# Performance work log

Hardware: AMD Instinct MI355X
Metric: run time of the kernel (lower is better)

## Reference

```python
import jax, jax.numpy as jnp
import numpy as np

SIM_T = 0.2       # similarity_threshold
AMB_T = 0.17      # ambiguous_threshold
SPLIT = 24576     # split_size
CAP = 65536       # fixed capacity per split for compacted pairs (padded with -1)


def _l2norm(x):
    # F.normalize(p=2, dim=1) with eps clamp
    n = jnp.linalg.norm(x, axis=1, keepdims=True)
    return x / jnp.maximum(n, 1e-12)


def setup_inputs():
    key = jax.random.key(0)
    ks = jax.random.split(key, 8)
    N1, N2, D = 4096, 49152, 512
    features = jax.random.normal(ks[0], (N1, D), dtype=jnp.float32)
    labels = jax.random.randint(ks[1], (N1,), 0, 10000, dtype=jnp.int32)
    counts = jax.random.randint(ks[2], (N1,), 0, 100, dtype=jnp.int32)
    indexes = jax.random.randint(ks[3], (N1,), 0, N2, dtype=jnp.int32)
    features_db = jax.random.normal(ks[4], (N2, D), dtype=jnp.float32)
    labels_db = jax.random.randint(ks[5], (N2,), 0, 10000, dtype=jnp.int32)
    counts_db = jax.random.randint(ks[6], (N2,), 0, 100, dtype=jnp.int32)
    indexes_db = jnp.arange(N2, dtype=jnp.int32)
    return {
        "features": features, "labels": labels, "counts": counts, "indexes": indexes,
        "features_db": features_db, "labels_db": labels_db,
        "counts_db": counts_db, "indexes_db": indexes_db,
    }


def reference(features, labels, counts, indexes,
              features_db, labels_db, counts_db, indexes_db):
    f1 = _l2norm(features)                        # [N1, D]
    f2 = _l2norm(features_db)                     # [N2, D]
    n_splits = features_db.shape[0] // SPLIT      # static small loop (2)
    ar = jnp.arange(CAP)
    similar_pairs, ambiguous_pairs = [], []
    for s in range(n_splits):
        sl = slice(s * SPLIT, (s + 1) * SPLIT)
        f2s, l2, c2, i2 = f2[sl], labels_db[sl], counts_db[sl], indexes_db[sl]
        sim = f1 @ f2s.T                          # [N1, SPLIT] cosine similarity
        # validity mask: global_idx1 < global_idx2 AND different labels
        valid = (indexes[:, None] < i2[None, :]) & (labels[:, None] != l2[None, :])
        # ---- similar pairs (sim > SIM_T) ----
        m = (sim > SIM_T) & valid
        r, c = jnp.nonzero(m, size=CAP, fill_value=0)   # fixed-size compaction
        good = ar < jnp.sum(m)
        p = jnp.stack([labels[r], l2[c]], axis=1)       # [CAP, 2] label pairs
        similar_pairs.append(jnp.where(good[:, None], p, -1))
        # ---- ambiguous pairs (AMB_T < sim < SIM_T), sorted by counts ----
        ma = (sim > AMB_T) & (sim < SIM_T) & valid
        r, c = jnp.nonzero(ma, size=CAP, fill_value=0)
        good = ar < jnp.sum(ma)
        p = jnp.stack([labels[r], l2[c]], axis=1)
        swap = counts[r] > c2[c]                        # argsort of 2-elem counts
        p = jnp.where(swap[:, None], p[:, ::-1], p)
        ambiguous_pairs.append(jnp.where(good[:, None], p, -1))
    similar_pairs = jnp.concatenate(similar_pairs, axis=0)     # [n_splits*CAP, 2]
    ambiguous_pairs = jnp.concatenate(ambiguous_pairs, axis=0) # [n_splits*CAP, 2]
    return similar_pairs, ambiguous_pairs
```

## Files before the change

kernel.cpp:

```cpp
#include <hip/hip_runtime.h>

typedef unsigned long long u64;

#define N1c 4096
#define N2c 49152
#define Dc 512
#define SPLITc 24576
#define NSPLITc 2
#define CAPc 65536
#define WPSc (SPLITc / 64)
#define SIM_Tc 0.2f
#define AMB_Tc 0.17f
#define DELTAc 0.01f
#define CANDMAX (1 << 20)

typedef __bf16 bf16x8 __attribute__((ext_vector_type(8)));
typedef float f32x4 __attribute__((ext_vector_type(4)));

static __device__ __forceinline__ unsigned short f2bf(float x) {
  unsigned u = __float_as_uint(x);
  unsigned r = (u + 0x7fffu + ((u >> 16) & 1u)) >> 16;
  return (unsigned short)r;
}

__global__ void sim_fill_out_k(int* __restrict__ out, int n, int* __restrict__ ccount) {
  int i = blockIdx.x * blockDim.x + threadIdx.x;
  if (i < n) out[i] = -1;
  if (i < NSPLITc) ccount[i] = 0;
}

__global__ void sim_norm_k(const float* __restrict__ f1, const float* __restrict__ f2,
                           float* __restrict__ invn, unsigned short* __restrict__ f1nb,
                           unsigned short* __restrict__ f2nb) {
  int wid = threadIdx.x >> 6, lane = threadIdx.x & 63;
  int row = blockIdx.x * 4 + wid;
  if (row >= N1c + N2c) return;
  const float* src = (row < N1c) ? (f1 + (size_t)row * Dc)
                                 : (f2 + (size_t)(row - N1c) * Dc);
  const float4* p = (const float4*)src;
  float4 v0 = p[lane];
  float4 v1 = p[lane + 64];
  float ss = v0.x*v0.x + v0.y*v0.y + v0.z*v0.z + v0.w*v0.w
           + v1.x*v1.x + v1.y*v1.y + v1.z*v1.z + v1.w*v1.w;
  #pragma unroll
  for (int d = 1; d < 64; d <<= 1) ss += __shfl_xor(ss, d);
  float inv = 1.0f / fmaxf(sqrtf(ss), 1e-12f);
  if (lane == 0) invn[row] = inv;
  unsigned short* dst = 0;
  if (row < N1c) dst = f1nb + (size_t)row * Dc;
  else if (row < N1c + SPLITc) dst = f2nb + (size_t)(row - N1c) * Dc;
  if (dst) {
    ushort4 o0, o1;
    o0.x = f2bf(v0.x*inv); o0.y = f2bf(v0.y*inv); o0.z = f2bf(v0.z*inv); o0.w = f2bf(v0.w*inv);
    o1.x = f2bf(v1.x*inv); o1.y = f2bf(v1.y*inv); o1.z = f2bf(v1.z*inv); o1.w = f2bf(v1.w*inv);
    ushort4* q = (ushort4*)dst;
    q[lane] = o0; q[lane + 64] = o1;
  }
}

__global__ void sim_conv2_k(const float* __restrict__ f2, const float* __restrict__ invn,
                            unsigned short* __restrict__ f2nb, int s) {
  int wid = threadIdx.x >> 6, lane = threadIdx.x & 63;
  int rloc = blockIdx.x * 4 + wid;
  if (rloc >= SPLITc) return;
  int grow = s * SPLITc + rloc;
  float inv = invn[N1c + grow];
  const float4* p = (const float4*)(f2 + (size_t)grow * Dc);
  float4 v0 = p[lane];
  float4 v1 = p[lane + 64];
  ushort4 o0, o1;
  o0.x = f2bf(v0.x*inv); o0.y = f2bf(v0.y*inv); o0.z = f2bf(v0.z*inv); o0.w = f2bf(v0.w*inv);
  o1.x = f2bf(v1.x*inv); o1.y = f2bf(v1.y*inv); o1.z = f2bf(v1.z*inv); o1.w = f2bf(v1.w*inv);
  ushort4* q = (ushort4*)(f2nb + (size_t)rloc * Dc);
  q[lane] = o0; q[lane + 64] = o1;
}

__global__ __launch_bounds__(256, 2) void sim_mfma_k(
    const unsigned short* __restrict__ Abf, const unsigned short* __restrict__ Bbf,
    const int* __restrict__ labels, const int* __restrict__ indexes,
    const int* __restrict__ labels_db, const int* __restrict__ indexes_db,
    u64* __restrict__ msim, u64* __restrict__ mamb,
    unsigned* __restrict__ cands, int* __restrict__ ccount, int s)
{
  __shared__ unsigned short As[128 * 64];
  __shared__ unsigned short Bs[128 * 64];
  __shared__ u64 wS[128][2];
  __shared__ u64 wA[128][2];
  __shared__ int meta[512];

  const int tid  = threadIdx.x;
  const int lane = tid & 63;
  const int wid  = tid >> 6;
  const int wm   = wid >> 1, wn = wid & 1;
  const int rbase = blockIdx.y * 128;
  const int bx   = blockIdx.x;
  const int cbase = ((bx & 7) * 24 + (bx >> 3)) * 128;

  {
    int r0 = tid & 127;
    bool hi = tid >= 128;
    int gcb = s * SPLITc + cbase;
    meta[tid]       = hi ? indexes[rbase + r0]    : labels[rbase + r0];
    meta[256 + tid] = hi ? indexes_db[gcb + r0]   : labels_db[gcb + r0];
  }

  f32x4 acc[4][4];
  #pragma unroll
  for (int i = 0; i < 4; ++i)
    #pragma unroll
    for (int j = 0; j < 4; ++j) acc[i][j] = (f32x4){0.f, 0.f, 0.f, 0.f};

  for (int kb = 0; kb < Dc; kb += 64) {
    __syncthreads();
    #pragma unroll
    for (int c4 = 0; c4 < 4; ++c4) {
      int c   = wid * 4 + c4;
      int row = c * 8 + (lane >> 3);
      int ls  = (lane & 7) ^ (row & 7);
      const unsigned short* ga = Abf + (size_t)(rbase + row) * Dc + kb + ls * 8;
      const unsigned short* gb = Bbf + (size_t)(cbase + row) * Dc + kb + ls * 8;
      __builtin_amdgcn_global_load_lds((const __attribute__((address_space(1))) void*)ga,
          (__attribute__((address_space(3))) void*)(As + c * 512), 16, 0, 0);
      __builtin_amdgcn_global_load_lds((const __attribute__((address_space(1))) void*)gb,
          (__attribute__((address_space(3))) void*)(Bs + c * 512), 16, 0, 0);
    }
    __syncthreads();
    #pragma unroll
    for (int kk = 0; kk < 2; ++kk) {
      bf16x8 a[4], b[4];
      #pragma unroll
      for (int mi = 0; mi < 4; ++mi) {
        int r  = wm * 64 + mi * 16 + (lane & 15);
        int ps = (kk * 4 + (lane >> 4)) ^ (r & 7);
        a[mi] = *(const bf16x8*)(const void*)(As + r * 64 + ps * 8);
      }
      #pragma unroll
      for (int ni = 0; ni < 4; ++ni) {
        int r  = wn * 64 + ni * 16 + (lane & 15);
        int ps = (kk * 4 + (lane >> 4)) ^ (r & 7);
        b[ni] = *(const bf16x8*)(const void*)(Bs + r * 64 + ps * 8);
      }
      #pragma unroll
      for (int mi = 0; mi < 4; ++mi)
        #pragma unroll
        for (int ni = 0; ni < 4; ++ni)
          acc[mi][ni] = __builtin_amdgcn_mfma_f32_16x16x32_bf16(a[mi], b[ni], acc[mi][ni], 0, 0, 0);
    }
  }

  wS[tid >> 1][tid & 1] = 0;
  wA[tid >> 1][tid & 1] = 0;
  __syncthreads();

  int lab2[4], idx2[4], cloc[4];
  #pragma unroll
  for (int ni = 0; ni < 4; ++ni) {
    int cl = wn * 64 + ni * 16 + (lane & 15);
    cloc[ni] = cbase + cl;
    lab2[ni] = meta[256 + cl];
    idx2[ni] = meta[384 + cl];
  }

  #pragma unroll
  for (int mi = 0; mi < 4; ++mi) {
    #pragma unroll
    for (int r = 0; r < 4; ++r) {
      int row128 = wm * 64 + mi * 16 + (lane >> 4) * 4 + r;
      int gr = rbase + row128;
      int lab1 = meta[row128], idx1 = meta[128 + row128];
      u64 sb = 0, ab = 0;
      #pragma unroll
      for (int ni = 0; ni < 4; ++ni) {
        float v = acc[mi][ni][r];
        if (idx1 < idx2[ni] && lab1 != lab2[ni]) {
          if (v > SIM_Tc + DELTAc) {
            sb |= 1ull << (ni * 16 + (lane & 15));
          } else if (v > AMB_Tc - DELTAc) {
            if (v < SIM_Tc - DELTAc && v > AMB_Tc + DELTAc) {
              ab |= 1ull << (ni * 16 + (lane & 15));
            } else {
              int ci = atomicAdd(ccount, 1);
              if (ci < CANDMAX)
                cands[ci] = ((unsigned)gr << 15) | (unsigned)cloc[ni];
            }
          }
        }
      }
      if (sb) atomicOr(&wS[row128][wn], sb);
      if (ab) atomicOr(&wA[row128][wn], ab);
    }
  }
  __syncthreads();
  {
    int row128 = tid >> 1, jh = tid & 1;
    size_t w = (size_t)(rbase + row128) * WPSc + (cbase >> 6) + jh;
    msim[w] = wS[row128][jh];
    mamb[w] = wA[row128][jh];
  }
}

__global__ void sim_recheck_k(const float* __restrict__ f1, const float* __restrict__ f2,
                              const float* __restrict__ invn,
                              const unsigned* __restrict__ cands, const int* __restrict__ ccount,
                              u64* __restrict__ msim, u64* __restrict__ mamb, int s) {
  int lane = threadIdx.x & 63;
  int gw = (blockIdx.x * blockDim.x + threadIdx.x) >> 6;
  int nw = (gridDim.x * blockDim.x) >> 6;
  int n = *ccount; if (n > CANDMAX) n = CANDMAX;
  for (int i = gw; i < n; i += nw) {
    unsigned pk = cands[i];
    int r = (int)(pk >> 15), c = (int)(pk & 0x7fffu);
    const float4* pa = (const float4*)(f1 + (size_t)r * Dc);
    const float4* pb = (const float4*)(f2 + ((size_t)s * SPLITc + c) * Dc);
    float4 a0 = pa[lane], a1 = pa[lane + 64];
    float4 b0 = pb[lane], b1 = pb[lane + 64];
    float d = a0.x*b0.x + a0.y*b0.y + a0.z*b0.z + a0.w*b0.w
            + a1.x*b1.x + a1.y*b1.y + a1.z*b1.z + a1.w*b1.w;
    #pragma unroll
    for (int t = 1; t < 64; t <<= 1) d += __shfl_xor(d, t);
    if (lane == 0) {
      float v = d * invn[r] * invn[N1c + s * SPLITc + c];
      if (v > SIM_Tc)
        atomicOr(&msim[(size_t)r * WPSc + (c >> 6)], 1ull << (c & 63));
      else if (v > AMB_Tc)
        atomicOr(&mamb[(size_t)r * WPSc + (c >> 6)], 1ull << (c & 63));
    }
  }
}

__global__ void sim_rowcount_k(const u64* __restrict__ msim, const u64* __restrict__ mamb,
                               int* __restrict__ rowcnt) {
  int row = blockIdx.x;
  int wid = threadIdx.x >> 6, lane = threadIdx.x & 63;
  const u64* m = wid ? mamb : msim;
  int ssum = 0;
  #pragma unroll
  for (int it = 0; it < WPSc / 64; ++it)
    ssum += __popcll(m[(size_t)row * WPSc + it * 64 + lane]);
  #pragma unroll
  for (int d = 32; d; d >>= 1) ssum += __shfl_down(ssum, d);
  if (lane == 0) rowcnt[wid * N1c + row] = ssum;
}

__global__ void sim_scan_k(const int* __restrict__ rowcnt, int* __restrict__ rowoff) {
  int cat = blockIdx.x;
  int tid = threadIdx.x;
  int v[16]; int ssum = 0;
  #pragma unroll
  for (int i = 0; i < 16; ++i) { v[i] = rowcnt[cat * N1c + tid * 16 + i]; ssum += v[i]; }
  int lane = tid & 63, wid = tid >> 6;
  int incl = ssum;
  #pragma unroll
  for (int d = 1; d < 64; d <<= 1) { int t = __shfl_up(incl, d); if (lane >= d) incl += t; }
  __shared__ int wsum[4];
  if (lane == 63) wsum[wid] = incl;
  __syncthreads();
  int woff = 0;
  for (int w = 0; w < wid; ++w) woff += wsum[w];
  int run = woff + incl - ssum;
  #pragma unroll
  for (int i = 0; i < 16; ++i) { rowoff[cat * N1c + tid * 16 + i] = run; run += v[i]; }
}

__global__ void sim_scatter_k(const u64* __restrict__ msim, const u64* __restrict__ mamb,
                              const int* __restrict__ rowoff,
                              const int* __restrict__ labels, const int* __restrict__ counts,
                              const int* __restrict__ labels_db, const int* __restrict__ counts_db,
                              int* __restrict__ out, int s) {
  int row = blockIdx.x;
  int cat = blockIdx.y;
  int lane = threadIdx.x;
  const u64* m = cat ? mamb : msim;
  int* o = out + (cat ? (NSPLITc * CAPc * 2 + s * CAPc * 2) : (s * CAPc * 2));
  int run = rowoff[cat * N1c + row];
  int lab1 = labels[row];
  int cnt1 = counts[row];
  for (int it = 0; it < WPSc / 64; ++it) {
    int w = it * 64 + lane;
    u64 x = m[(size_t)row * WPSc + w];
    int pc = __popcll(x);
    int incl = pc;
    #pragma unroll
    for (int d = 1; d < 64; d <<= 1) { int t = __shfl_up(incl, d); if (lane >= d) incl += t; }
    int pos = run + incl - pc;
    int tot = __shfl(incl, 63);
    while (x) {
      int b = __builtin_ctzll(x);
      x &= x - 1;
      if (pos < CAPc) {
        int gc = s * SPLITc + w * 64 + b;
        int l2v = labels_db[gc];
        if (cat == 0) {
          o[2 * pos]     = lab1;
          o[2 * pos + 1] = l2v;
        } else {
          bool sw = cnt1 > counts_db[gc];
          o[2 * pos]     = sw ? l2v : lab1;
          o[2 * pos + 1] = sw ? lab1 : l2v;
        }
      }
      ++pos;
    }
    run += tot;
  }
}

extern "C" void kernel_launch(void* const* d_in, const int* in_sizes, int n_in,
                              void* d_out, int out_size, void* d_ws, size_t ws_size,
                              hipStream_t stream) {
  const float* features    = (const float*)d_in[0];
  const int*   labels      = (const int*)  d_in[1];
  const int*   counts      = (const int*)  d_in[2];
  const int*   indexes     = (const int*)  d_in[3];
  const float* features_db = (const float*)d_in[4];
  const int*   labels_db   = (const int*)  d_in[5];
  const int*   counts_db   = (const int*)  d_in[6];
  const int*   indexes_db  = (const int*)  d_in[7];
  int* out = (int*)d_out;

  u64*   msim   = (u64*)d_ws;
  u64*   mamb   = msim + (size_t)N1c * WPSc;
  float* invn   = (float*)(mamb + (size_t)N1c * WPSc);
  int*   rowcnt = (int*)(invn + (N1c + N2c));
  int*   rowoff = rowcnt + 2 * N1c;
  int*   ccount = rowoff + 2 * N1c;
  unsigned* cands = (unsigned*)(ccount + 4);
  unsigned short* f1nb = (unsigned short*)(cands + CANDMAX);
  unsigned short* f2nb = f1nb + (size_t)N1c * Dc;

  sim_fill_out_k<<<(out_size + 255) / 256, 256, 0, stream>>>(out, out_size, ccount);
  sim_norm_k<<<(N1c + N2c + 3) / 4, 256, 0, stream>>>(features, features_db, invn, f1nb, f2nb);

  for (int s = 0; s < NSPLITc; ++s) {
    if (s) sim_conv2_k<<<SPLITc / 4, 256, 0, stream>>>(features_db, invn, f2nb, s);
    sim_mfma_k<<<dim3(SPLITc / 128, N1c / 128), 256, 0, stream>>>(
        f1nb, f2nb, labels, indexes, labels_db, indexes_db,
        msim, mamb, cands, ccount + s, s);
    sim_recheck_k<<<512, 256, 0, stream>>>(features, features_db, invn,
                                           cands, ccount + s, msim, mamb, s);
    sim_rowcount_k<<<N1c, 128, 0, stream>>>(msim, mamb, rowcnt);
    sim_scan_k<<<2, 256, 0, stream>>>(rowcnt, rowoff);
    sim_scatter_k<<<dim3(N1c, 2), 64, 0, stream>>>(
        msim, mamb, rowoff, labels, counts, labels_db, counts_db, out, s);
  }
}
```

Measured before the change: 360.4 us.

## Switch similarity GEMM to int8 MFMA with per-row scales and error bounds

```diff
diff --git a/kernel.cpp b/kernel.cpp
--- a/kernel.cpp
+++ b/kernel.cpp
@@ -11,17 +11,9 @@
 #define WPSc (SPLITc / 64)
 #define SIM_Tc 0.2f
 #define AMB_Tc 0.17f
-#define DELTAc 0.01f
 #define CANDMAX (1 << 20)
 
-typedef __bf16 bf16x8 __attribute__((ext_vector_type(8)));
-typedef float f32x4 __attribute__((ext_vector_type(4)));
-
-static __device__ __forceinline__ unsigned short f2bf(float x) {
-  unsigned u = __float_as_uint(x);
-  unsigned r = (u + 0x7fffu + ((u >> 16) & 1u)) >> 16;
-  return (unsigned short)r;
-}
+typedef int i32x4 __attribute__((ext_vector_type(4)));
 
 __global__ void sim_fill_out_k(int* __restrict__ out, int n, int* __restrict__ ccount) {
   int i = blockIdx.x * blockDim.x + threadIdx.x;
@@ -29,9 +21,9 @@
   if (i < NSPLITc) ccount[i] = 0;
 }
 
-__global__ void sim_norm_k(const float* __restrict__ f1, const float* __restrict__ f2,
-                           float* __restrict__ invn, unsigned short* __restrict__ f1nb,
-                           unsigned short* __restrict__ f2nb) {
+__global__ void sim_quant_k(const float* __restrict__ f1, const float* __restrict__ f2,
+                            float* __restrict__ invn, signed char* __restrict__ f1q,
+                            signed char* __restrict__ f2q, float2* __restrict__ qmeta) {
   int wid = threadIdx.x >> 6, lane = threadIdx.x & 63;
   int row = blockIdx.x * 4 + wid;
   if (row >= N1c + N2c) return;
@@ -45,48 +37,49 @@
   #pragma unroll
   for (int d = 1; d < 64; d <<= 1) ss += __shfl_xor(ss, d);
   float inv = 1.0f / fmaxf(sqrtf(ss), 1e-12f);
-  if (lane == 0) invn[row] = inv;
-  unsigned short* dst = 0;
-  if (row < N1c) dst = f1nb + (size_t)row * Dc;
-  else if (row < N1c + SPLITc) dst = f2nb + (size_t)(row - N1c) * Dc;
-  if (dst) {
-    ushort4 o0, o1;
-    o0.x = f2bf(v0.x*inv); o0.y = f2bf(v0.y*inv); o0.z = f2bf(v0.z*inv); o0.w = f2bf(v0.w*inv);
-    o1.x = f2bf(v1.x*inv); o1.y = f2bf(v1.y*inv); o1.z = f2bf(v1.z*inv); o1.w = f2bf(v1.w*inv);
-    ushort4* q = (ushort4*)dst;
-    q[lane] = o0; q[lane + 64] = o1;
-  }
-}
-
-__global__ void sim_conv2_k(const float* __restrict__ f2, const float* __restrict__ invn,
-                            unsigned short* __restrict__ f2nb, int s) {
-  int wid = threadIdx.x >> 6, lane = threadIdx.x & 63;
-  int rloc = blockIdx.x * 4 + wid;
-  if (rloc >= SPLITc) return;
-  int grow = s * SPLITc + rloc;
-  float inv = invn[N1c + grow];
-  const float4* p = (const float4*)(f2 + (size_t)grow * Dc);
-  float4 v0 = p[lane];
-  float4 v1 = p[lane + 64];
-  ushort4 o0, o1;
-  o0.x = f2bf(v0.x*inv); o0.y = f2bf(v0.y*inv); o0.z = f2bf(v0.z*inv); o0.w = f2bf(v0.w*inv);
-  o1.x = f2bf(v1.x*inv); o1.y = f2bf(v1.y*inv); o1.z = f2bf(v1.z*inv); o1.w = f2bf(v1.w*inv);
-  ushort4* q = (ushort4*)(f2nb + (size_t)rloc * Dc);
-  q[lane] = o0; q[lane + 64] = o1;
+  float n[8] = {v0.x*inv, v0.y*inv, v0.z*inv, v0.w*inv,
+                v1.x*inv, v1.y*inv, v1.z*inv, v1.w*inv};
+  float m = 0.f;
+  #pragma unroll
+  for (int j = 0; j < 8; ++j) m = fmaxf(m, fabsf(n[j]));
+  #pragma unroll
+  for (int d = 1; d < 64; d <<= 1) m = fmaxf(m, __shfl_xor(m, d));
+  float q  = fmaxf(m, 1e-30f) * (1.0f / 127.0f);
+  float rq = 1.0f / q;
+  int iq[8], l1 = 0;
+  #pragma unroll
+  for (int j = 0; j < 8; ++j) {
+    int t = (int)rintf(n[j] * rq);
+    t = max(-127, min(127, t));
+    iq[j] = t; l1 += abs(t);
+  }
+  #pragma unroll
+  for (int d = 1; d < 64; d <<= 1) l1 += __shfl_xor(l1, d);
+  signed char* dst = (row < N1c) ? (f1q + (size_t)row * Dc)
+                                 : (f2q + (size_t)(row - N1c) * Dc);
+  char4 c0; c0.x = (signed char)iq[0]; c0.y = (signed char)iq[1];
+            c0.z = (signed char)iq[2]; c0.w = (signed char)iq[3];
+  char4 c1; c1.x = (signed char)iq[4]; c1.y = (signed char)iq[5];
+            c1.z = (signed char)iq[6]; c1.w = (signed char)iq[7];
+  ((char4*)dst)[lane]      = c0;
+  ((char4*)dst)[lane + 64] = c1;
+  if (lane == 0) { invn[row] = inv; qmeta[row] = make_float2(q, q * (float)l1); }
 }
 
 __global__ __launch_bounds__(256, 2) void sim_mfma_k(
-    const unsigned short* __restrict__ Abf, const unsigned short* __restrict__ Bbf,
+    const signed char* __restrict__ Aq, const signed char* __restrict__ Bq,
     const int* __restrict__ labels, const int* __restrict__ indexes,
     const int* __restrict__ labels_db, const int* __restrict__ indexes_db,
+    const float2* __restrict__ qmeta,
     u64* __restrict__ msim, u64* __restrict__ mamb,
     unsigned* __restrict__ cands, int* __restrict__ ccount, int s)
 {
-  __shared__ unsigned short As[128 * 64];
-  __shared__ unsigned short Bs[128 * 64];
+  __shared__ __align__(16) signed char As[128 * 128];
+  __shared__ __align__(16) signed char Bs[128 * 128];
   __shared__ u64 wS[128][2];
   __shared__ u64 wA[128][2];
-  __shared__ int meta[512];
+  __shared__ int   meta[512];
+  __shared__ float fmeta[512];
 
   const int tid  = threadIdx.x;
   const int lane = tid & 63;
@@ -95,56 +88,63 @@
   const int rbase = blockIdx.y * 128;
   const int bx   = blockIdx.x;
   const int cbase = ((bx & 7) * 24 + (bx >> 3)) * 128;
+  const int gcb   = s * SPLITc + cbase;
 
   {
     int r0 = tid & 127;
     bool hi = tid >= 128;
-    int gcb = s * SPLITc + cbase;
-    meta[tid]       = hi ? indexes[rbase + r0]    : labels[rbase + r0];
-    meta[256 + tid] = hi ? indexes_db[gcb + r0]   : labels_db[gcb + r0];
-  }
-
-  f32x4 acc[4][4];
+    meta[tid]       = hi ? indexes[rbase + r0]  : labels[rbase + r0];
+    meta[256 + tid] = hi ? indexes_db[gcb + r0] : labels_db[gcb + r0];
+    if (!hi) {
+      float2 mr = qmeta[rbase + r0];
+      fmeta[r0] = mr.x; fmeta[128 + r0] = mr.y;
+    } else {
+      float2 mc = qmeta[N1c + gcb + r0];
+      fmeta[256 + r0] = mc.x; fmeta[384 + r0] = mc.y;
+    }
+  }
+
+  i32x4 acc[4][4];
   #pragma unroll
   for (int i = 0; i < 4; ++i)
     #pragma unroll
-    for (int j = 0; j < 4; ++j) acc[i][j] = (f32x4){0.f, 0.f, 0.f, 0.f};
-
-  for (int kb = 0; kb < Dc; kb += 64) {
+    for (int j = 0; j < 4; ++j) acc[i][j] = (i32x4){0, 0, 0, 0};
+
+  for (int kb = 0; kb < Dc; kb += 128) {
     __syncthreads();
     #pragma unroll
     for (int c4 = 0; c4 < 4; ++c4) {
       int c   = wid * 4 + c4;
       int row = c * 8 + (lane >> 3);
       int ls  = (lane & 7) ^ (row & 7);
-      const unsigned short* ga = Abf + (size_t)(rbase + row) * Dc + kb + ls * 8;
-      const unsigned short* gb = Bbf + (size_t)(cbase + row) * Dc + kb + ls * 8;
+      const signed char* ga = Aq + (size_t)(rbase + row) * Dc + kb + ls * 16;
+      const signed char* gb = Bq + (size_t)(gcb + row) * Dc + kb + ls * 16;
       __builtin_amdgcn_global_load_lds((const __attribute__((address_space(1))) void*)ga,
-          (__attribute__((address_space(3))) void*)(As + c * 512), 16, 0, 0);
+          (__attribute__((address_space(3))) void*)(As + c * 1024), 16, 0, 0);
       __builtin_amdgcn_global_load_lds((const __attribute__((address_space(1))) void*)gb,
-          (__attribute__((address_space(3))) void*)(Bs + c * 512), 16, 0, 0);
+          (__attribute__((address_space(3))) void*)(Bs + c * 1024), 16, 0, 0);
     }
     __syncthreads();
     #pragma unroll
     for (int kk = 0; kk < 2; ++kk) {
-      bf16x8 a[4], b[4];
+      i32x4 a[4], b[4];
       #pragma unroll
       for (int mi = 0; mi < 4; ++mi) {
         int r  = wm * 64 + mi * 16 + (lane & 15);
         int ps = (kk * 4 + (lane >> 4)) ^ (r & 7);
-        a[mi] = *(const bf16x8*)(const void*)(As + r * 64 + ps * 8);
+        a[mi] = *(const i32x4*)(const void*)(As + r * 128 + ps * 16);
       }
       #pragma unroll
       for (int ni = 0; ni < 4; ++ni) {
         int r  = wn * 64 + ni * 16 + (lane & 15);
         int ps = (kk * 4 + (lane >> 4)) ^ (r & 7);
-        b[ni] = *(const bf16x8*)(const void*)(Bs + r * 64 + ps * 8);
+        b[ni] = *(const i32x4*)(const void*)(Bs + r * 128 + ps * 16);
       }
       #pragma unroll
       for (int mi = 0; mi < 4; ++mi)
         #pragma unroll
         for (int ni = 0; ni < 4; ++ni)
-          acc[mi][ni] = __builtin_amdgcn_mfma_f32_16x16x32_bf16(a[mi], b[ni], acc[mi][ni], 0, 0, 0);
+          acc[mi][ni] = __builtin_amdgcn_mfma_i32_16x16x64_i8(a[mi], b[ni], acc[mi][ni], 0, 0, 0);
     }
   }
 
@@ -152,13 +152,15 @@
   wA[tid >> 1][tid & 1] = 0;
   __syncthreads();
 
-  int lab2[4], idx2[4], cloc[4];
+  int lab2[4], idx2[4], cloc[4]; float qb_[4], sb_[4];
   #pragma unroll
   for (int ni = 0; ni < 4; ++ni) {
     int cl = wn * 64 + ni * 16 + (lane & 15);
     cloc[ni] = cbase + cl;
     lab2[ni] = meta[256 + cl];
     idx2[ni] = meta[384 + cl];
+    qb_[ni]  = fmeta[256 + cl];
+    sb_[ni]  = fmeta[384 + cl];
   }
 
   #pragma unroll
@@ -168,15 +170,17 @@
       int row128 = wm * 64 + mi * 16 + (lane >> 4) * 4 + r;
       int gr = rbase + row128;
       int lab1 = meta[row128], idx1 = meta[128 + row128];
+      float qa = fmeta[row128], sa = fmeta[128 + row128];
       u64 sb = 0, ab = 0;
       #pragma unroll
       for (int ni = 0; ni < 4; ++ni) {
-        float v = acc[mi][ni][r];
+        float v   = (float)acc[mi][ni][r] * (qa * qb_[ni]);
+        float bnd = 0.5f * (qa * sb_[ni] + qb_[ni] * sa) + 128.f * (qa * qb_[ni]) + 1e-3f;
         if (idx1 < idx2[ni] && lab1 != lab2[ni]) {
-          if (v > SIM_Tc + DELTAc) {
+          if (v > SIM_Tc + bnd) {
             sb |= 1ull << (ni * 16 + (lane & 15));
-          } else if (v > AMB_Tc - DELTAc) {
-            if (v < SIM_Tc - DELTAc && v > AMB_Tc + DELTAc) {
+          } else if (v > AMB_Tc - bnd) {
+            if (v < SIM_Tc - bnd && v > AMB_Tc + bnd) {
               ab |= 1ull << (ni * 16 + (lane & 15));
             } else {
               int ci = atomicAdd(ccount, 1);
@@ -325,16 +329,17 @@
   int*   rowoff = rowcnt + 2 * N1c;
   int*   ccount = rowoff + 2 * N1c;
   unsigned* cands = (unsigned*)(ccount + 4);
-  unsigned short* f1nb = (unsigned short*)(cands + CANDMAX);
-  unsigned short* f2nb = f1nb + (size_t)N1c * Dc;
+  float2* qmeta = (float2*)(cands + CANDMAX);
+  signed char* f1q = (signed char*)(qmeta + (N1c + N2c));
+  signed char* f2q = f1q + (size_t)N1c * Dc;
 
   sim_fill_out_k<<<(out_size + 255) / 256, 256, 0, stream>>>(out, out_size, ccount);
-  sim_norm_k<<<(N1c + N2c + 3) / 4, 256, 0, stream>>>(features, features_db, invn, f1nb, f2nb);
+  sim_quant_k<<<(N1c + N2c + 3) / 4, 256, 0, stream>>>(features, features_db,
+                                                       invn, f1q, f2q, qmeta);
 
   for (int s = 0; s < NSPLITc; ++s) {
-    if (s) sim_conv2_k<<<SPLITc / 4, 256, 0, stream>>>(features_db, invn, f2nb, s);
     sim_mfma_k<<<dim3(SPLITc / 128, N1c / 128), 256, 0, stream>>>(
-        f1nb, f2nb, labels, indexes, labels_db, indexes_db,
+        f1q, f2q, labels, indexes, labels_db, indexes_db, qmeta,
         msim, mamb, cands, ccount + s, s);
     sim_recheck_k<<<512, 256, 0, stream>>>(features, features_db, invn,
                                            cands, ccount + s, msim, mamb, s);
```

Result: slower. 572.9 us (+59.0%).
